# Performance work log

Measured on AMD Instinct MI355X. Metric: run time of the kernel, lower is better.

## Reference

```python
import jax, jax.numpy as jnp
import numpy as np

NUM_HEADS = 8
LN_EPS = 1e-5


def _layernorm(t, w, b):
    mu = t.mean(-1, keepdims=True)
    var = t.var(-1, keepdims=True)  # ddof=0, matches torch LayerNorm
    return (t - mu) * jax.lax.rsqrt(var + LN_EPS) * w + b


def setup_inputs() -> dict:
    key = jax.random.key(0)
    ks = jax.random.split(key, 5)
    B, C, H, W = 16, 384, 32, 32
    hidden = 4 * C
    s = 0.02
    return {
        "x": jax.random.normal(ks[0], (B, C, H, W), jnp.float32),
        "ln1_w": jnp.ones((C,), jnp.float32),
        "ln1_b": jnp.zeros((C,), jnp.float32),
        "qkv_w": s * jax.random.normal(ks[1], (3 * C, C), jnp.float32),
        "qkv_b": jnp.zeros((3 * C,), jnp.float32),
        "proj_w": s * jax.random.normal(ks[2], (C, C), jnp.float32),
        "proj_b": jnp.zeros((C,), jnp.float32),
        "ln2_w": jnp.ones((C,), jnp.float32),
        "ln2_b": jnp.zeros((C,), jnp.float32),
        "fc1_w": s * jax.random.normal(ks[3], (hidden, C), jnp.float32),
        "fc1_b": jnp.zeros((hidden,), jnp.float32),
        "fc2_w": s * jax.random.normal(ks[4], (C, hidden), jnp.float32),
        "fc2_b": jnp.zeros((C,), jnp.float32),
    }


def reference(x, ln1_w, ln1_b, qkv_w, qkv_b, proj_w, proj_b,
              ln2_w, ln2_b, fc1_w, fc1_b, fc2_w, fc2_b):
    B, C, H, W = x.shape
    N = H * W
    nh = NUM_HEADS
    hd = C // nh
    scale = hd ** (-0.5)

    xf = x.reshape(B, C, N).transpose(0, 2, 1)  # (B, N, C) tokens

    # --- pre-norm attention ---
    h1 = _layernorm(xf, ln1_w, ln1_b)
    qkv = h1 @ qkv_w.T + qkv_b                      # (B, N, 3C)
    qkv = qkv.reshape(B, N, 3, nh, hd).transpose(2, 0, 3, 1, 4)  # (3,B,h,N,d)
    q, k, v = qkv[0], qkv[1], qkv[2]
    attn = jax.nn.softmax(jnp.einsum('bhnd,bhmd->bhnm', q, k) * scale, axis=-1)
    out = jnp.einsum('bhnm,bhmd->bhnd', attn, v)    # (B,h,N,d)
    out = out.transpose(0, 2, 1, 3).reshape(B, N, C)
    out = out @ proj_w.T + proj_b
    xf = xf + out

    # --- pre-norm FFN (exact GELU, matching torch nn.GELU default) ---
    h2 = _layernorm(xf, ln2_w, ln2_b)
    f = jax.nn.gelu(h2 @ fc1_w.T + fc1_b, approximate=False)
    f = f @ fc2_w.T + fc2_b
    xf = xf + f

    return xf.transpose(0, 2, 1).reshape(B, C, H, W)
```

## Files before the change

### kernel.cpp

```cpp
#include <hip/hip_runtime.h>

typedef unsigned short u16;
using bf16x8 = __attribute__((ext_vector_type(8))) short;
using f32x4  = __attribute__((ext_vector_type(4))) float;

#define DEV __device__ __forceinline__

constexpr int    NTOK = 16384;
constexpr size_t QKSZ = (size_t)16 * 8 * 1024 * 64;
constexpr float  ATTN_SCALE = 0.14433756729740645f;

DEV u16 f2bf(float x) {
  unsigned int u = __float_as_uint(x);
  u += 0x7fffu + ((u >> 16) & 1u);
  return (u16)(u >> 16);
}

DEV void async16(const u16* g, u16* l) {
  __builtin_amdgcn_global_load_lds(
      (const __attribute__((address_space(1))) unsigned int*)g,
      (__attribute__((address_space(3))) unsigned int*)l, 16, 0, 0);
}

DEV const bf16x8* lds_swz(const u16* base, int row, int bytecol) {
  int byte = row * 128 + bytecol;
  byte ^= (row & 7) << 4;
  return (const bf16x8*)((const char*)base + byte);
}

DEV float gelu_f(float x) {
  float y = 0.7978845608028654f * (x + 0.044715f * x * x * x);
  float e = __expf(2.f * y);
  float t = 1.f - 2.f / (e + 1.f);
  return 0.5f * x * (1.f + t);
}

__global__ void cvt_kernel(const float* __restrict__ qkvw, const float* __restrict__ qkvb,
                           const float* __restrict__ projw, const float* __restrict__ fc1w,
                           const float* __restrict__ fc2w,
                           u16* __restrict__ wqkvp, float* __restrict__ biasp,
                           u16* __restrict__ wproj, u16* __restrict__ wfc1,
                           u16* __restrict__ wfc2) {
  int i = blockIdx.x * 256 + threadIdx.x;
  if (i < 147456) {
    int p = i / 96, q = (i - p * 96) * 4;
    int which = p >> 9, h = (p >> 6) & 7, d = p & 63;
    ushort4 o{0, 0, 0, 0};
    if (d < 48) {
      float sc = which ? 1.f : ATTN_SCALE;
      float4 v = *(const float4*)(qkvw + (size_t)(which * 384 + h * 48 + d) * 384 + q);
      o = ushort4{f2bf(v.x * sc), f2bf(v.y * sc), f2bf(v.z * sc), f2bf(v.w * sc)};
    }
    *(ushort4*)(wqkvp + (size_t)p * 384 + q) = o;
  } else if (i < 479232) {
    const float* s; u16* d; int off;
    if (i < 184320)      { s = projw; d = wproj; off = i - 147456; }
    else if (i < 331776) { s = fc1w;  d = wfc1;  off = i - 184320; }
    else                 { s = fc2w;  d = wfc2;  off = i - 331776; }
    float4 v = *(const float4*)(s + (size_t)off * 4);
    *(ushort4*)(d + (size_t)off * 4) = ushort4{f2bf(v.x), f2bf(v.y), f2bf(v.z), f2bf(v.w)};
  } else if (i < 479616) {
    int qi = (i - 479232) * 4;
    float4 o;
    float* op = (float*)&o;
#pragma unroll
    for (int r = 0; r < 4; ++r) {
      int p = qi + r, which = p >> 9, h = (p >> 6) & 7, d = p & 63;
      op[r] = (d < 48) ? qkvb[which * 384 + h * 48 + d] * (which ? 1.f : ATTN_SCALE) : 0.f;
    }
    *(float4*)(biasp + qi) = o;
  }
}

__global__ __launch_bounds__(256) void ln_kernel(
    const float* __restrict__ in, const float* __restrict__ gw,
    const float* __restrict__ gb, u16* __restrict__ out) {
  __shared__ float tile[32][385];
  __shared__ float mu_s[32], rs_s[32];
  const int b = blockIdx.y;
  const int n0 = blockIdx.x * 32;
  const int t = threadIdx.x;
  const int j = t & 31, cb = t >> 5;
  const float* src = in + (size_t)b * 384 * 1024 + n0;
  for (int k = 0; k < 48; ++k) {
    int c = k * 8 + cb;
    tile[j][c] = src[(size_t)c * 1024 + j];
  }
  __syncthreads();
  const int jt = t >> 3, r = t & 7;
  float s = 0.f, ss = 0.f;
  for (int c = r; c < 384; c += 8) { float v = tile[jt][c]; s += v; ss += v * v; }
  s += __shfl_xor(s, 1); ss += __shfl_xor(ss, 1);
  s += __shfl_xor(s, 2); ss += __shfl_xor(ss, 2);
  s += __shfl_xor(s, 4); ss += __shfl_xor(ss, 4);
  const float mean = s * (1.f / 384.f);
  const float var  = ss * (1.f / 384.f) - mean * mean;
  if (r == 0) { mu_s[jt] = mean; rs_s[jt] = rsqrtf(var + 1e-5f); }
  __syncthreads();
  for (int q = t; q < 3072; q += 256) {
    int tok = q / 96, c4 = (q - tok * 96) * 4;
    float m = mu_s[tok], rv = rs_s[tok];
    float4 wv = *(const float4*)(gw + c4);
    float4 bv = *(const float4*)(gb + c4);
    u16* dst = out + (size_t)(b * 1024 + n0 + tok) * 384 + c4;
    ushort4 o{f2bf((tile[tok][c4 + 0] - m) * rv * wv.x + bv.x),
              f2bf((tile[tok][c4 + 1] - m) * rv * wv.y + bv.y),
              f2bf((tile[tok][c4 + 2] - m) * rv * wv.z + bv.z),
              f2bf((tile[tok][c4 + 3] - m) * rv * wv.w + bv.w)};
    *(ushort4*)dst = o;
  }
}

template<int EPI>
__global__ __launch_bounds__(256, 3) void gemm_kernel(
    const u16* __restrict__ A, const u16* __restrict__ W,
    const float* __restrict__ bias, float* __restrict__ outf,
    u16* __restrict__ outh, const float* __restrict__ resid, int K) {
  constexpr bool SWAP = (EPI == 0 || EPI == 2);
  __shared__ u16 sA[3][4096], sB[3][4096];
  const int m0 = blockIdx.x * 128;
  const int n0 = (EPI == 4 ? 1024 : 0) + blockIdx.y * 128;
  const int wv = threadIdx.x >> 6, lane = threadIdx.x & 63;
  const int wm = (wv >> 1) * 64, wn = (wv & 1) * 64;
  const int l16 = lane & 15, lg = lane >> 4;
  const int rsw = (lg ^ (l16 & 3)) << 4;

  f32x4 acc[4][4];
#pragma unroll
  for (int i = 0; i < 4; ++i)
#pragma unroll
    for (int jj = 0; jj < 4; ++jj) acc[i][jj] = f32x4{0.f, 0.f, 0.f, 0.f};

  const int nk = K >> 5;
  auto stage = [&](int buf, int kt) {
    const u16* Ab = A + (size_t)m0 * K + kt * 32;
    const u16* Wb = W + (size_t)n0 * K + kt * 32;
#pragma unroll
    for (int i = 0; i < 2; ++i) {
      int chunk = i * 256 + wv * 64 + lane;
      int row = chunk >> 2, sl = (chunk & 3) ^ (row & 3);
      async16(Ab + (size_t)row * K + sl * 8, &sA[buf][(i * 256 + wv * 64) * 8]);
      async16(Wb + (size_t)row * K + sl * 8, &sB[buf][(i * 256 + wv * 64) * 8]);
    }
  };
  stage(0, 0);
  stage(1, 1);
  int buf = 0;
  for (int kt = 0; kt < nk; ++kt) {
    if (kt < nk - 1) asm volatile("s_waitcnt vmcnt(4)" ::: "memory");
    else             asm volatile("s_waitcnt vmcnt(0)" ::: "memory");
    __builtin_amdgcn_s_barrier();
    if (kt + 2 < nk) { int nb = buf + 2; if (nb >= 3) nb -= 3; stage(nb, kt + 2); }
    bf16x8 av[4], bv[4];
#pragma unroll
    for (int f = 0; f < 4; ++f) {
      av[f] = *(const bf16x8*)((const char*)&sA[buf][0] + (wm + f * 16 + l16) * 64 + rsw);
      bv[f] = *(const bf16x8*)((const char*)&sB[buf][0] + (wn + f * 16 + l16) * 64 + rsw);
    }
    __builtin_amdgcn_s_setprio(1);
#pragma unroll
    for (int mf = 0; mf < 4; ++mf)
#pragma unroll
      for (int nf = 0; nf < 4; ++nf) {
        if constexpr (SWAP)
          acc[mf][nf] = __builtin_amdgcn_mfma_f32_16x16x32_bf16(bv[nf], av[mf], acc[mf][nf], 0, 0, 0);
        else
          acc[mf][nf] = __builtin_amdgcn_mfma_f32_16x16x32_bf16(av[mf], bv[nf], acc[mf][nf], 0, 0, 0);
      }
    __builtin_amdgcn_s_setprio(0);
    ++buf; if (buf >= 3) buf = 0;
  }

  if constexpr (SWAP) {
#pragma unroll
    for (int mf = 0; mf < 4; ++mf) {
      const int token = m0 + wm + mf * 16 + l16;
      const int b = token >> 10, nn = token & 1023;
#pragma unroll
      for (int nf = 0; nf < 4; ++nf) {
        const int col = n0 + wn + nf * 16 + lg * 4;
        f32x4 v = acc[mf][nf];
        float4 bb = *(const float4*)(bias + col);
        unsigned long long pk = 0;
        if constexpr (EPI == 0) {
#pragma unroll
          for (int rr = 0; rr < 4; ++rr)
            pk |= (unsigned long long)f2bf(v[rr] + ((const float*)&bb)[rr]) << (16 * rr);
          const int which = col >> 9, h = (col >> 6) & 7, d0 = col & 63;
          size_t idx = (size_t)which * QKSZ + (size_t)((b * 8 + h) * 1024 + nn) * 64 + d0;
          *(unsigned long long*)&outh[idx] = pk;
        } else {
#pragma unroll
          for (int rr = 0; rr < 4; ++rr)
            pk |= (unsigned long long)f2bf(gelu_f(v[rr] + ((const float*)&bb)[rr])) << (16 * rr);
          *(unsigned long long*)&outh[(size_t)token * 1536 + col] = pk;
        }
      }
    }
  } else {
#pragma unroll
    for (int mf = 0; mf < 4; ++mf) {
      const int mm = m0 + wm + mf * 16 + lg * 4;
      const int b = mm >> 10, nn = mm & 1023;
#pragma unroll
      for (int nf = 0; nf < 4; ++nf) {
        const int col = n0 + wn + nf * 16 + l16;
        f32x4 v = acc[mf][nf];
        const float bs = bias[col];
        if constexpr (EPI == 4) {
          unsigned long long pk = 0;
#pragma unroll
          for (int rr = 0; rr < 4; ++rr)
            pk |= (unsigned long long)f2bf(v[rr] + bs) << (16 * rr);
          const int h = (col >> 6) & 7, d = col & 63;
          size_t idx = 2ull * QKSZ + (((size_t)((b * 8 + h) * 64 + d)) << 10) + nn;
          *(unsigned long long*)&outh[idx] = pk;
        } else {
          size_t idx = ((size_t)(b * 384 + col) << 10) + nn;
          float4 rr4 = *(const float4*)&resid[idx];
          float4 o{v[0] + bs + rr4.x, v[1] + bs + rr4.y, v[2] + bs + rr4.z, v[3] + bs + rr4.w};
          *(float4*)&outf[idx] = o;
        }
      }
    }
  }
}

__global__ __launch_bounds__(256, 2) void attn_kernel(
    const u16* __restrict__ Qg, const u16* __restrict__ Kg,
    const u16* __restrict__ Vtg, u16* __restrict__ outp) {
  __shared__ u16 Ks[3][4096];
  __shared__ u16 Vs[3][4096];
  __shared__ u16 QPs[4 * 32 * 72];
  const int orig = blockIdx.x;
  const int swz = (orig & 7) * 128 + (orig >> 3);
  const int bh = swz >> 3, qt = swz & 7;
  const int w = threadIdx.x >> 6, lane = threadIdx.x & 63;
  const int l16 = lane & 15, lg = lane >> 4;

  const u16* kbase = Kg + (size_t)bh * 1024 * 64;
  const u16* vbase = Vtg + (size_t)bh * 64 * 1024;

  auto stageKV = [&](int buf, int kv) {
#pragma unroll
    for (int i = 0; i < 2; ++i) {
      int cb = (i * 4 + w) * 64;
      int ck = cb + lane;
      int g  = ck ^ ((ck >> 3) & 7);
      async16(kbase + (size_t)kv * 4096 + g * 8, &Ks[buf][cb * 8]);
      async16(vbase + (size_t)(g >> 3) * 1024 + kv * 64 + (g & 7) * 8, &Vs[buf][cb * 8]);
    }
  };

  {
    const u16* src = Qg + (size_t)(bh * 1024 + qt * 128) * 64;
#pragma unroll
    for (int i = 0; i < 4; ++i) {
      int cb = (i * 4 + w) * 64;
      int ck = cb + lane;
      int g  = ck ^ ((ck >> 3) & 7);
      async16(src + g * 8, &QPs[cb * 8]);
    }
  }
  stageKV(0, 0);
  stageKV(1, 1);
  asm volatile("s_waitcnt vmcnt(8)" ::: "memory");
  __builtin_amdgcn_s_barrier();

  bf16x8 qf[2][2];
#pragma unroll
  for (int mf = 0; mf < 2; ++mf)
#pragma unroll
    for (int ks = 0; ks < 2; ++ks)
      qf[mf][ks] = *lds_swz(QPs, w * 32 + mf * 16 + l16, ks * 64 + lg * 16);
  asm volatile("s_waitcnt lgkmcnt(0)" ::: "memory");
  __builtin_amdgcn_s_barrier();

  float lr[2][4];
  f32x4 acco[2][4];
#pragma unroll
  for (int mf = 0; mf < 2; ++mf) {
#pragma unroll
    for (int r = 0; r < 4; ++r) lr[mf][r] = 0.f;
#pragma unroll
    for (int df = 0; df < 4; ++df) acco[mf][df] = f32x4{0.f, 0.f, 0.f, 0.f};
  }
  u16* Pw = &QPs[w * 32 * 72];

  auto compute = [&](int buf) {
    f32x4 accs[2][4];
#pragma unroll
    for (int mf = 0; mf < 2; ++mf)
#pragma unroll
      for (int nf = 0; nf < 4; ++nf) accs[mf][nf] = f32x4{0.f, 0.f, 0.f, 0.f};
    __builtin_amdgcn_s_setprio(1);
#pragma unroll
    for (int nf = 0; nf < 4; ++nf) {
      bf16x8 k0 = *lds_swz(Ks[buf], nf * 16 + l16, lg * 16);
      bf16x8 k1 = *lds_swz(Ks[buf], nf * 16 + l16, 64 + lg * 16);
#pragma unroll
      for (int mf = 0; mf < 2; ++mf) {
        accs[mf][nf] = __builtin_amdgcn_mfma_f32_16x16x32_bf16(qf[mf][0], k0, accs[mf][nf], 0, 0, 0);
        accs[mf][nf] = __builtin_amdgcn_mfma_f32_16x16x32_bf16(qf[mf][1], k1, accs[mf][nf], 0, 0, 0);
      }
    }
    __builtin_amdgcn_s_setprio(0);
#pragma unroll
    for (int mf = 0; mf < 2; ++mf)
#pragma unroll
      for (int r = 0; r < 4; ++r) {
        float s0 = __expf(accs[mf][0][r]);
        float s1 = __expf(accs[mf][1][r]);
        float s2 = __expf(accs[mf][2][r]);
        float s3 = __expf(accs[mf][3][r]);
        accs[mf][0][r] = s0; accs[mf][1][r] = s1;
        accs[mf][2][r] = s2; accs[mf][3][r] = s3;
        lr[mf][r] += s0 + s1 + s2 + s3;
      }
#pragma unroll
    for (int mf = 0; mf < 2; ++mf)
#pragma unroll
      for (int nf = 0; nf < 4; ++nf)
#pragma unroll
        for (int r = 0; r < 4; ++r)
          Pw[(mf * 16 + lg * 4 + r) * 72 + nf * 16 + l16] = f2bf(accs[mf][nf][r]);
    asm volatile("s_waitcnt lgkmcnt(0)" ::: "memory");
#pragma unroll
    for (int ks = 0; ks < 2; ++ks) {
      bf16x8 pa[2], vf[4];
#pragma unroll
      for (int mf = 0; mf < 2; ++mf)
        pa[mf] = *(const bf16x8*)&Pw[(mf * 16 + l16) * 72 + ks * 32 + lg * 8];
#pragma unroll
      for (int df = 0; df < 4; ++df)
        vf[df] = *lds_swz(Vs[buf], df * 16 + l16, ks * 64 + lg * 16);
      __builtin_amdgcn_s_setprio(1);
#pragma unroll
      for (int mf = 0; mf < 2; ++mf)
#pragma unroll
        for (int df = 0; df < 4; ++df)
          acco[mf][df] = __builtin_amdgcn_mfma_f32_16x16x32_bf16(pa[mf], vf[df], acco[mf][df], 0, 0, 0);
      __builtin_amdgcn_s_setprio(0);
    }
  };

  int buf = 0;
  for (int kv = 0; kv < 16; ++kv) {
    if (kv < 15) asm volatile("s_waitcnt vmcnt(4)" ::: "memory");
    else         asm volatile("s_waitcnt vmcnt(0)" ::: "memory");
    __builtin_amdgcn_s_barrier();
    if (kv + 2 < 16) { int nb = buf + 2; if (nb >= 3) nb -= 3; stageKV(nb, kv + 2); }
    compute(buf);
    ++buf; if (buf >= 3) buf = 0;
  }

  const int b = bh >> 3, h = bh & 7;
#pragma unroll
  for (int mf = 0; mf < 2; ++mf)
#pragma unroll
    for (int r = 0; r < 4; ++r) {
      float t = lr[mf][r];
      t += __shfl_xor(t, 1); t += __shfl_xor(t, 2);
      t += __shfl_xor(t, 4); t += __shfl_xor(t, 8);
      float inv = 1.f / t;
      int token = qt * 128 + w * 32 + mf * 16 + lg * 4 + r;
      size_t rowb = (size_t)(b * 1024 + token) * 384 + h * 48;
#pragma unroll
      for (int df = 0; df < 3; ++df)
        outp[rowb + df * 16 + l16] = f2bf(acco[mf][df][r] * inv);
    }
}

constexpr size_t OFF_WQKVP = 0;
constexpr size_t OFF_BIASP = 1179648;
constexpr size_t OFF_WPROJ = 1185792;
constexpr size_t OFF_WFC1  = 1480704;
constexpr size_t OFF_WFC2  = 2660352;
constexpr size_t OFF_H     = 3840000;
constexpr size_t OFF_QKV   = 16422912;
constexpr size_t OFF_AO    = 66754560;
constexpr size_t OFF_Y1T   = 79337472;

extern "C" void kernel_launch(void* const* d_in, const int* in_sizes, int n_in,
                              void* d_out, int out_size, void* d_ws, size_t ws_size,
                              hipStream_t stream) {
  (void)in_sizes; (void)n_in; (void)out_size; (void)ws_size;
  const float* x     = (const float*)d_in[0];
  const float* ln1w  = (const float*)d_in[1];
  const float* ln1b  = (const float*)d_in[2];
  const float* qkvw  = (const float*)d_in[3];
  const float* qkvbi = (const float*)d_in[4];
  const float* projw = (const float*)d_in[5];
  const float* projb = (const float*)d_in[6];
  const float* ln2w  = (const float*)d_in[7];
  const float* ln2b  = (const float*)d_in[8];
  const float* fc1w  = (const float*)d_in[9];
  const float* fc1b  = (const float*)d_in[10];
  const float* fc2w  = (const float*)d_in[11];
  const float* fc2b  = (const float*)d_in[12];

  char* ws = (char*)d_ws;
  u16*   wqkvp = (u16*)(ws + OFF_WQKVP);
  float* biasp = (float*)(ws + OFF_BIASP);
  u16*   wproj = (u16*)(ws + OFF_WPROJ);
  u16*   wfc1  = (u16*)(ws + OFF_WFC1);
  u16*   wfc2  = (u16*)(ws + OFF_WFC2);
  u16*   h1    = (u16*)(ws + OFF_H);
  u16*   qkvs  = (u16*)(ws + OFF_QKV);
  u16*   f1    = qkvs;
  u16*   ao    = (u16*)(ws + OFF_AO);
  float* y1t   = (float*)(ws + OFF_Y1T);

  cvt_kernel<<<1874, 256, 0, stream>>>(qkvw, qkvbi, projw, fc1w, fc2w,
                                       wqkvp, biasp, wproj, wfc1, wfc2);

  dim3 lngrid(32, 16);
  ln_kernel<<<lngrid, 256, 0, stream>>>(x, ln1w, ln1b, h1);

  gemm_kernel<0><<<dim3(NTOK / 128, 8), 256, 0, stream>>>(h1, wqkvp, biasp, nullptr, qkvs, nullptr, 384);
  gemm_kernel<4><<<dim3(NTOK / 128, 4), 256, 0, stream>>>(h1, wqkvp, biasp, nullptr, qkvs, nullptr, 384);

  attn_kernel<<<dim3(1024), 256, 0, stream>>>(qkvs, qkvs + QKSZ, qkvs + 2 * QKSZ, ao);

  gemm_kernel<1><<<dim3(NTOK / 128, 3), 256, 0, stream>>>(ao, wproj, projb, y1t, nullptr, x, 384);

  ln_kernel<<<lngrid, 256, 0, stream>>>(y1t, ln2w, ln2b, h1 );

  gemm_kernel<2><<<dim3(NTOK / 128, 12), 256, 0, stream>>>(h1, wfc1, fc1b, nullptr, f1, nullptr, 384);

  gemm_kernel<3><<<dim3(NTOK / 128, 3), 256, 0, stream>>>(f1, wfc2, fc2b, (float*)d_out, nullptr, y1t, 1536);
}
```

Before: 320.9 us.

## Add 256x256 GEMM tile for QK and FC1, switch pipelines to double-buffered BK=64

Adds a 512-thread GEMM kernel with 256x256 output tiles and BK=64 for the Q/K projection and the FC1+GELU GEMM, which raises operand reuse per LDS load. The remaining 128x128 GEMM moves from a 3-stage BK=32 ring to a 2-stage BK=64 double buffer with an 8-way XOR swizzle. The attention kernel also drops from triple to double buffering so occupancy can go to 3 blocks. The risks are shallower prefetch depth that exposes load latency, and a 256x256 grid with fewer blocks than the GPU has CUs (256 and 384), which hurts load balance.

```diff
diff --git a/kernel.cpp b/kernel.cpp
--- a/kernel.cpp
+++ b/kernel.cpp
@@ -112,18 +112,105 @@
 }
 
 template<int EPI>
-__global__ __launch_bounds__(256, 3) void gemm_kernel(
+__global__ __launch_bounds__(512, 2) void gemm256_kernel(
+    const u16* __restrict__ A, const u16* __restrict__ W,
+    const float* __restrict__ bias, u16* __restrict__ outh, int K) {
+  __shared__ u16 sA[2][16384], sB[2][16384];
+  const int m0 = blockIdx.x * 256, n0 = blockIdx.y * 256;
+  const int tid = threadIdx.x;
+  const int wv = tid >> 6, lane = tid & 63;
+  const int wm = (wv >> 2) * 128, wn = (wv & 3) * 64;
+  const int l16 = lane & 15, lg = lane >> 4;
+  const int ksw = (l16 & 7) << 4;
+
+  f32x4 acc[8][4];
+#pragma unroll
+  for (int i = 0; i < 8; ++i)
+#pragma unroll
+    for (int jj = 0; jj < 4; ++jj) acc[i][jj] = f32x4{0.f, 0.f, 0.f, 0.f};
+
+  const int nk = K >> 6;
+  auto stage = [&](int buf, int kt) {
+    const u16* Ab = A + (size_t)m0 * K + kt * 64;
+    const u16* Wb = W + (size_t)n0 * K + kt * 64;
+#pragma unroll
+    for (int j = 0; j < 4; ++j) {
+      int cb = j * 512 + wv * 64;
+      int c = cb + lane;
+      int row = c >> 3, sl = (c & 7) ^ (row & 7);
+      async16(Ab + (size_t)row * K + sl * 8, &sA[buf][cb * 8]);
+      async16(Wb + (size_t)row * K + sl * 8, &sB[buf][cb * 8]);
+    }
+  };
+  stage(0, 0);
+  int buf = 0;
+  for (int kt = 0; kt < nk; ++kt) {
+    asm volatile("s_waitcnt vmcnt(0)" ::: "memory");
+    __builtin_amdgcn_s_barrier();
+    if (kt + 1 < nk) stage(buf ^ 1, kt + 1);
+#pragma unroll
+    for (int ks = 0; ks < 2; ++ks) {
+      bf16x8 av[8], bv[4];
+#pragma unroll
+      for (int f = 0; f < 4; ++f) {
+        int rb = wn + f * 16 + l16;
+        bv[f] = *(const bf16x8*)((const char*)&sB[buf][0] + rb * 128 + ((ks * 64 + lg * 16) ^ ksw));
+      }
+#pragma unroll
+      for (int f = 0; f < 8; ++f) {
+        int ra = wm + f * 16 + l16;
+        av[f] = *(const bf16x8*)((const char*)&sA[buf][0] + ra * 128 + ((ks * 64 + lg * 16) ^ ksw));
+      }
+      __builtin_amdgcn_s_setprio(1);
+#pragma unroll
+      for (int mf = 0; mf < 8; ++mf)
+#pragma unroll
+        for (int nf = 0; nf < 4; ++nf)
+          acc[mf][nf] = __builtin_amdgcn_mfma_f32_16x16x32_bf16(bv[nf], av[mf], acc[mf][nf], 0, 0, 0);
+      __builtin_amdgcn_s_setprio(0);
+    }
+    buf ^= 1;
+  }
+
+#pragma unroll
+  for (int mf = 0; mf < 8; ++mf) {
+    const int token = m0 + wm + mf * 16 + l16;
+    const int b = token >> 10, nn = token & 1023;
+#pragma unroll
+    for (int nf = 0; nf < 4; ++nf) {
+      const int col = n0 + wn + nf * 16 + lg * 4;
+      f32x4 v = acc[mf][nf];
+      float4 bb = *(const float4*)(bias + col);
+      unsigned long long pk = 0;
+      if constexpr (EPI == 0) {
+#pragma unroll
+        for (int rr = 0; rr < 4; ++rr)
+          pk |= (unsigned long long)f2bf(v[rr] + ((const float*)&bb)[rr]) << (16 * rr);
+        const int which = col >> 9, h = (col >> 6) & 7, d0 = col & 63;
+        size_t idx = (size_t)which * QKSZ + (size_t)((b * 8 + h) * 1024 + nn) * 64 + d0;
+        *(unsigned long long*)&outh[idx] = pk;
+      } else {
+#pragma unroll
+        for (int rr = 0; rr < 4; ++rr)
+          pk |= (unsigned long long)f2bf(gelu_f(v[rr] + ((const float*)&bb)[rr])) << (16 * rr);
+        *(unsigned long long*)&outh[(size_t)token * 1536 + col] = pk;
+      }
+    }
+  }
+}
+
+template<int EPI>
+__global__ __launch_bounds__(256, 2) void gemm_kernel(
     const u16* __restrict__ A, const u16* __restrict__ W,
     const float* __restrict__ bias, float* __restrict__ outf,
     u16* __restrict__ outh, const float* __restrict__ resid, int K) {
-  constexpr bool SWAP = (EPI == 0 || EPI == 2);
-  __shared__ u16 sA[3][4096], sB[3][4096];
+  __shared__ u16 sA[2][8192], sB[2][8192];
   const int m0 = blockIdx.x * 128;
   const int n0 = (EPI == 4 ? 1024 : 0) + blockIdx.y * 128;
   const int wv = threadIdx.x >> 6, lane = threadIdx.x & 63;
   const int wm = (wv >> 1) * 64, wn = (wv & 1) * 64;
   const int l16 = lane & 15, lg = lane >> 4;
-  const int rsw = (lg ^ (l16 & 3)) << 4;
+  const int ksw = (l16 & 7) << 4;
 
   f32x4 acc[4][4];
 #pragma unroll
@@ -131,106 +218,77 @@
 #pragma unroll
     for (int jj = 0; jj < 4; ++jj) acc[i][jj] = f32x4{0.f, 0.f, 0.f, 0.f};
 
-  const int nk = K >> 5;
+  const int nk = K >> 6;
   auto stage = [&](int buf, int kt) {
-    const u16* Ab = A + (size_t)m0 * K + kt * 32;
-    const u16* Wb = W + (size_t)n0 * K + kt * 32;
-#pragma unroll
-    for (int i = 0; i < 2; ++i) {
-      int chunk = i * 256 + wv * 64 + lane;
-      int row = chunk >> 2, sl = (chunk & 3) ^ (row & 3);
-      async16(Ab + (size_t)row * K + sl * 8, &sA[buf][(i * 256 + wv * 64) * 8]);
-      async16(Wb + (size_t)row * K + sl * 8, &sB[buf][(i * 256 + wv * 64) * 8]);
+    const u16* Ab = A + (size_t)m0 * K + kt * 64;
+    const u16* Wb = W + (size_t)n0 * K + kt * 64;
+#pragma unroll
+    for (int j = 0; j < 4; ++j) {
+      int cb = j * 256 + wv * 64;
+      int c = cb + lane;
+      int row = c >> 3, sl = (c & 7) ^ (row & 7);
+      async16(Ab + (size_t)row * K + sl * 8, &sA[buf][cb * 8]);
+      async16(Wb + (size_t)row * K + sl * 8, &sB[buf][cb * 8]);
     }
   };
   stage(0, 0);
-  stage(1, 1);
   int buf = 0;
   for (int kt = 0; kt < nk; ++kt) {
-    if (kt < nk - 1) asm volatile("s_waitcnt vmcnt(4)" ::: "memory");
-    else             asm volatile("s_waitcnt vmcnt(0)" ::: "memory");
+    asm volatile("s_waitcnt vmcnt(0)" ::: "memory");
     __builtin_amdgcn_s_barrier();
-    if (kt + 2 < nk) { int nb = buf + 2; if (nb >= 3) nb -= 3; stage(nb, kt + 2); }
-    bf16x8 av[4], bv[4];
-#pragma unroll
-    for (int f = 0; f < 4; ++f) {
-      av[f] = *(const bf16x8*)((const char*)&sA[buf][0] + (wm + f * 16 + l16) * 64 + rsw);
-      bv[f] = *(const bf16x8*)((const char*)&sB[buf][0] + (wn + f * 16 + l16) * 64 + rsw);
-    }
-    __builtin_amdgcn_s_setprio(1);
-#pragma unroll
-    for (int mf = 0; mf < 4; ++mf)
-#pragma unroll
-      for (int nf = 0; nf < 4; ++nf) {
-        if constexpr (SWAP)
-          acc[mf][nf] = __builtin_amdgcn_mfma_f32_16x16x32_bf16(bv[nf], av[mf], acc[mf][nf], 0, 0, 0);
-        else
+    if (kt + 1 < nk) stage(buf ^ 1, kt + 1);
+#pragma unroll
+    for (int ks = 0; ks < 2; ++ks) {
+      bf16x8 av[4], bv[4];
+#pragma unroll
+      for (int f = 0; f < 4; ++f) {
+        int ra = wm + f * 16 + l16, rb = wn + f * 16 + l16;
+        av[f] = *(const bf16x8*)((const char*)&sA[buf][0] + ra * 128 + ((ks * 64 + lg * 16) ^ ksw));
+        bv[f] = *(const bf16x8*)((const char*)&sB[buf][0] + rb * 128 + ((ks * 64 + lg * 16) ^ ksw));
+      }
+      __builtin_amdgcn_s_setprio(1);
+#pragma unroll
+      for (int mf = 0; mf < 4; ++mf)
+#pragma unroll
+        for (int nf = 0; nf < 4; ++nf)
           acc[mf][nf] = __builtin_amdgcn_mfma_f32_16x16x32_bf16(av[mf], bv[nf], acc[mf][nf], 0, 0, 0);
-      }
-    __builtin_amdgcn_s_setprio(0);
-    ++buf; if (buf >= 3) buf = 0;
-  }
-
-  if constexpr (SWAP) {
-#pragma unroll
-    for (int mf = 0; mf < 4; ++mf) {
-      const int token = m0 + wm + mf * 16 + l16;
-      const int b = token >> 10, nn = token & 1023;
-#pragma unroll
-      for (int nf = 0; nf < 4; ++nf) {
-        const int col = n0 + wn + nf * 16 + lg * 4;
-        f32x4 v = acc[mf][nf];
-        float4 bb = *(const float4*)(bias + col);
+      __builtin_amdgcn_s_setprio(0);
+    }
+    buf ^= 1;
+  }
+
+#pragma unroll
+  for (int mf = 0; mf < 4; ++mf) {
+    const int mm = m0 + wm + mf * 16 + lg * 4;
+    const int b = mm >> 10, nn = mm & 1023;
+#pragma unroll
+    for (int nf = 0; nf < 4; ++nf) {
+      const int col = n0 + wn + nf * 16 + l16;
+      f32x4 v = acc[mf][nf];
+      const float bs = bias[col];
+      if constexpr (EPI == 4) {
         unsigned long long pk = 0;
-        if constexpr (EPI == 0) {
-#pragma unroll
-          for (int rr = 0; rr < 4; ++rr)
-            pk |= (unsigned long long)f2bf(v[rr] + ((const float*)&bb)[rr]) << (16 * rr);
-          const int which = col >> 9, h = (col >> 6) & 7, d0 = col & 63;
-          size_t idx = (size_t)which * QKSZ + (size_t)((b * 8 + h) * 1024 + nn) * 64 + d0;
-          *(unsigned long long*)&outh[idx] = pk;
-        } else {
-#pragma unroll
-          for (int rr = 0; rr < 4; ++rr)
-            pk |= (unsigned long long)f2bf(gelu_f(v[rr] + ((const float*)&bb)[rr])) << (16 * rr);
-          *(unsigned long long*)&outh[(size_t)token * 1536 + col] = pk;
-        }
-      }
-    }
-  } else {
-#pragma unroll
-    for (int mf = 0; mf < 4; ++mf) {
-      const int mm = m0 + wm + mf * 16 + lg * 4;
-      const int b = mm >> 10, nn = mm & 1023;
-#pragma unroll
-      for (int nf = 0; nf < 4; ++nf) {
-        const int col = n0 + wn + nf * 16 + l16;
-        f32x4 v = acc[mf][nf];
-        const float bs = bias[col];
-        if constexpr (EPI == 4) {
-          unsigned long long pk = 0;
-#pragma unroll
-          for (int rr = 0; rr < 4; ++rr)
-            pk |= (unsigned long long)f2bf(v[rr] + bs) << (16 * rr);
-          const int h = (col >> 6) & 7, d = col & 63;
-          size_t idx = 2ull * QKSZ + (((size_t)((b * 8 + h) * 64 + d)) << 10) + nn;
-          *(unsigned long long*)&outh[idx] = pk;
-        } else {
-          size_t idx = ((size_t)(b * 384 + col) << 10) + nn;
-          float4 rr4 = *(const float4*)&resid[idx];
-          float4 o{v[0] + bs + rr4.x, v[1] + bs + rr4.y, v[2] + bs + rr4.z, v[3] + bs + rr4.w};
-          *(float4*)&outf[idx] = o;
-        }
-      }
-    }
-  }
-}
-
-__global__ __launch_bounds__(256, 2) void attn_kernel(
+#pragma unroll
+        for (int rr = 0; rr < 4; ++rr)
+          pk |= (unsigned long long)f2bf(v[rr] + bs) << (16 * rr);
+        const int h = (col >> 6) & 7, d = col & 63;
+        size_t idx = 2ull * QKSZ + (((size_t)((b * 8 + h) * 64 + d)) << 10) + nn;
+        *(unsigned long long*)&outh[idx] = pk;
+      } else {
+        size_t idx = ((size_t)(b * 384 + col) << 10) + nn;
+        float4 rr4 = *(const float4*)&resid[idx];
+        float4 o{v[0] + bs + rr4.x, v[1] + bs + rr4.y, v[2] + bs + rr4.z, v[3] + bs + rr4.w};
+        *(float4*)&outf[idx] = o;
+      }
+    }
+  }
+}
+
+__global__ __launch_bounds__(256, 3) void attn_kernel(
     const u16* __restrict__ Qg, const u16* __restrict__ Kg,
     const u16* __restrict__ Vtg, u16* __restrict__ outp) {
-  __shared__ u16 Ks[3][4096];
-  __shared__ u16 Vs[3][4096];
+  __shared__ u16 Ks[2][4096];
+  __shared__ u16 Vs[2][4096];
   __shared__ u16 QPs[4 * 32 * 72];
   const int orig = blockIdx.x;
   const int swz = (orig & 7) * 128 + (orig >> 3);
@@ -263,8 +321,7 @@
     }
   }
   stageKV(0, 0);
-  stageKV(1, 1);
-  asm volatile("s_waitcnt vmcnt(8)" ::: "memory");
+  asm volatile("s_waitcnt vmcnt(0)" ::: "memory");
   __builtin_amdgcn_s_barrier();
 
   bf16x8 qf[2][2];
@@ -346,12 +403,11 @@
 
   int buf = 0;
   for (int kv = 0; kv < 16; ++kv) {
-    if (kv < 15) asm volatile("s_waitcnt vmcnt(4)" ::: "memory");
-    else         asm volatile("s_waitcnt vmcnt(0)" ::: "memory");
+    if (kv + 1 < 16) stageKV(buf ^ 1, kv + 1);
+    compute(buf);
+    asm volatile("s_waitcnt vmcnt(0)" ::: "memory");
     __builtin_amdgcn_s_barrier();
-    if (kv + 2 < 16) { int nb = buf + 2; if (nb >= 3) nb -= 3; stageKV(nb, kv + 2); }
-    compute(buf);
-    ++buf; if (buf >= 3) buf = 0;
+    buf ^= 1;
   }
 
   const int b = bh >> 3, h = bh & 7;
@@ -417,16 +473,16 @@
   dim3 lngrid(32, 16);
   ln_kernel<<<lngrid, 256, 0, stream>>>(x, ln1w, ln1b, h1);
 
-  gemm_kernel<0><<<dim3(NTOK / 128, 8), 256, 0, stream>>>(h1, wqkvp, biasp, nullptr, qkvs, nullptr, 384);
-  gemm_kernel<4><<<dim3(NTOK / 128, 4), 256, 0, stream>>>(h1, wqkvp, biasp, nullptr, qkvs, nullptr, 384);
+  gemm256_kernel<0><<<dim3(64, 4), 512, 0, stream>>>(h1, wqkvp, biasp, qkvs, 384);
+  gemm_kernel<4><<<dim3(128, 4), 256, 0, stream>>>(h1, wqkvp, biasp, nullptr, qkvs, nullptr, 384);
 
   attn_kernel<<<dim3(1024), 256, 0, stream>>>(qkvs, qkvs + QKSZ, qkvs + 2 * QKSZ, ao);
 
-  gemm_kernel<1><<<dim3(NTOK / 128, 3), 256, 0, stream>>>(ao, wproj, projb, y1t, nullptr, x, 384);
+  gemm_kernel<1><<<dim3(128, 3), 256, 0, stream>>>(ao, wproj, projb, y1t, nullptr, x, 384);
 
   ln_kernel<<<lngrid, 256, 0, stream>>>(y1t, ln2w, ln2b, h1 );
 
-  gemm_kernel<2><<<dim3(NTOK / 128, 12), 256, 0, stream>>>(h1, wfc1, fc1b, nullptr, f1, nullptr, 384);
-
-  gemm_kernel<3><<<dim3(NTOK / 128, 3), 256, 0, stream>>>(f1, wfc2, fc2b, (float*)d_out, nullptr, y1t, 1536);
-}
+  gemm256_kernel<2><<<dim3(64, 6), 512, 0, stream>>>(h1, wfc1, fc1b, f1, 384);
+
+  gemm_kernel<3><<<dim3(128, 3), 256, 0, stream>>>(f1, wfc2, fc2b, (float*)d_out, nullptr, y1t, 1536);
+}
```

New measurement: 317.7 us. Within noise of the previous version (-1.0%).
